# Kernel tuning notes

Hardware: AMD Instinct MI355X
Metric: run time of the kernel (lower is better)

Reference implementation:

```python
import jax, jax.numpy as jnp
import numpy as np

C = 192
B, H, W = 16, 64, 64
FILTERS = (1, 3, 3, 3, 1)
INIT_SCALE = 10.0
LIKELIHOOD_BOUND = 1e-6


def setup_inputs() -> dict:
    key = jax.random.key(0)
    kx, *kb = jax.random.split(key, 6)
    x = jax.random.normal(kx, (B, C, H, W), dtype=jnp.float32)
    scale = INIT_SCALE ** (1.0 / (len(FILTERS) - 1))
    inp = {"x": x}
    for i in range(4):
        init = float(np.log(np.expm1(1.0 / scale / FILTERS[i + 1])))
        inp[f"m{i}"] = jnp.full((C, FILTERS[i + 1], FILTERS[i]), init, dtype=jnp.float32)
        inp[f"b{i}"] = jax.random.uniform(kb[i], (C, FILTERS[i + 1], 1), minval=-0.5, maxval=0.5, dtype=jnp.float32)
    for i in range(3):
        inp[f"f{i}"] = jnp.zeros((C, FILTERS[i + 1], 1), dtype=jnp.float32)
    return inp


def _logits_cumulative(logits, mats, biases, factors):
    # logits: (C, 1, N); mats[i]: (C, f_out, f_in)
    for i in range(len(mats)):
        m = jax.nn.softplus(mats[i])
        logits = jnp.einsum('coi,cin->con', m, logits) + biases[i]
        if i < len(factors):
            logits = logits + jnp.tanh(factors[i]) * jnp.tanh(logits)
    return logits


def reference(x, m0, m1, m2, m3, b0, b1, b2, b3, f0, f1, f2):
    mats = (m0, m1, m2, m3)
    biases = (b0, b1, b2, b3)
    factors = (f0, f1, f2)
    b, c, h, w = x.shape
    xt = jnp.transpose(x, (1, 0, 2, 3)).reshape(c, 1, -1)  # (C,1,N)
    lower = _logits_cumulative(xt - 0.5, mats, biases, factors)
    upper = _logits_cumulative(xt + 0.5, mats, biases, factors)
    sign = jax.lax.stop_gradient(-jnp.sign(lower + upper))
    likelihood = jnp.abs(jax.nn.sigmoid(sign * upper) - jax.nn.sigmoid(sign * lower))
    likelihood = jnp.maximum(likelihood, LIKELIHOOD_BOUND)  # Low_bound forward = clamp
    likelihood = likelihood.reshape(c, b, h, w)
    return jnp.transpose(likelihood, (1, 0, 2, 3))
```

## Files before the change

kernel.cpp:

```cpp
#include <hip/hip_runtime.h>
#include <cmath>

#define NCH 192
#define SLAB 4096
#define LUT_N 512
#define LUT_XMIN (-8.0f)
#define LUT_H (16.0f / (float)LUT_N)
#define LUT_INVH ((float)LUT_N / 16.0f)
#define LUT_OFF (-(LUT_XMIN) * LUT_INVH)
#define SLABS_PER_BLOCK 4

typedef float f4_t __attribute__((ext_vector_type(4)));

__device__ __forceinline__ float sigmoidf_(float x) {
    return 1.0f / (1.0f + __expf(-x));
}

__device__ __forceinline__ float softplusf_(float x) {
    return (x > 20.0f) ? x : log1pf(expf(x));
}

__device__ __forceinline__ float mlp_eval(const float* __restrict__ p, float z,
                                          bool g0, bool g1, bool g2) {
    float t0 = fmaf(p[0], z, p[24]);
    float t1 = fmaf(p[1], z, p[25]);
    float t2 = fmaf(p[2], z, p[26]);
    if (g0) {
        t0 += p[34] * tanhf(t0);
        t1 += p[35] * tanhf(t1);
        t2 += p[36] * tanhf(t2);
    }
    float u0 = fmaf(p[3], t0, fmaf(p[4], t1, fmaf(p[5], t2, p[27])));
    float u1 = fmaf(p[6], t0, fmaf(p[7], t1, fmaf(p[8], t2, p[28])));
    float u2 = fmaf(p[9], t0, fmaf(p[10], t1, fmaf(p[11], t2, p[29])));
    if (g1) {
        u0 += p[37] * tanhf(u0);
        u1 += p[38] * tanhf(u1);
        u2 += p[39] * tanhf(u2);
    }
    float w0 = fmaf(p[12], u0, fmaf(p[13], u1, fmaf(p[14], u2, p[30])));
    float w1 = fmaf(p[15], u0, fmaf(p[16], u1, fmaf(p[17], u2, p[31])));
    float w2 = fmaf(p[18], u0, fmaf(p[19], u1, fmaf(p[20], u2, p[32])));
    if (g2) {
        w0 += p[40] * tanhf(w0);
        w1 += p[41] * tanhf(w1);
        w2 += p[42] * tanhf(w2);
    }
    return fmaf(p[21], w0, fmaf(p[22], w1, fmaf(p[23], w2, p[33])));
}

__device__ __forceinline__ float element(const float* __restrict__ p, float v,
                                         bool g0, bool g1, bool g2) {
    float lo = mlp_eval(p, v - 0.5f, g0, g1, g2);
    float up = mlp_eval(p, v + 0.5f, g0, g1, g2);
    float ssum = lo + up;
    float s = (ssum > 0.0f) ? -1.0f : ((ssum < 0.0f) ? 1.0f : 0.0f);
    float lk = fabsf(sigmoidf_(s * up) - sigmoidf_(s * lo));
    return fmaxf(lk, 1e-6f);
}

__device__ __forceinline__ void stage_params(
    float* p, int c, int tid,
    const float* __restrict__ m0, const float* __restrict__ b0,
    const float* __restrict__ m1, const float* __restrict__ b1,
    const float* __restrict__ m2, const float* __restrict__ b2,
    const float* __restrict__ m3, const float* __restrict__ b3,
    const float* __restrict__ f0, const float* __restrict__ f1,
    const float* __restrict__ f2)
{
    if (tid < 43) {
        float v;
        if (tid < 3)       v = softplusf_(m0[c * 3 + tid]);
        else if (tid < 12) v = softplusf_(m1[c * 9 + (tid - 3)]);
        else if (tid < 21) v = softplusf_(m2[c * 9 + (tid - 12)]);
        else if (tid < 24) v = softplusf_(m3[c * 3 + (tid - 21)]);
        else if (tid < 27) v = b0[c * 3 + (tid - 24)];
        else if (tid < 30) v = b1[c * 3 + (tid - 27)];
        else if (tid < 33) v = b2[c * 3 + (tid - 30)];
        else if (tid < 34) v = b3[c];
        else if (tid < 37) v = tanhf(f0[c * 3 + (tid - 34)]);
        else if (tid < 40) v = tanhf(f1[c * 3 + (tid - 37)]);
        else               v = tanhf(f2[c * 3 + (tid - 40)]);
        p[tid] = v;
    }
}

__global__ __launch_bounds__(256) void eb_fused_kernel(
    const float* __restrict__ x,
    const float* __restrict__ m0, const float* __restrict__ b0,
    const float* __restrict__ m1, const float* __restrict__ b1,
    const float* __restrict__ m2, const float* __restrict__ b2,
    const float* __restrict__ m3, const float* __restrict__ b3,
    const float* __restrict__ f0, const float* __restrict__ f1,
    const float* __restrict__ f2,
    float* __restrict__ out)
{
    __shared__ float p[43];
    __shared__ float f[LUT_N + 1];

    const int c   = blockIdx.x >> 2;
    const int q   = blockIdx.x & 3;
    const int tid = threadIdx.x;

    stage_params(p, c, tid, m0, b0, m1, b1, m2, b2, m3, b3, f0, f1, f2);
    __syncthreads();

    const bool g0 = (p[34] != 0.0f) | (p[35] != 0.0f) | (p[36] != 0.0f);
    const bool g1 = (p[37] != 0.0f) | (p[38] != 0.0f) | (p[39] != 0.0f);
    const bool g2 = (p[40] != 0.0f) | (p[41] != 0.0f) | (p[42] != 0.0f);

    float4 v[SLABS_PER_BLOCK * 4];
    size_t bases[SLABS_PER_BLOCK];
#pragma unroll
    for (int s = 0; s < SLABS_PER_BLOCK; ++s) {
        const int b = q * SLABS_PER_BLOCK + s;
        bases[s] = ((size_t)b * NCH + c) * SLAB;
        const float4* __restrict__ xin = (const float4*)(x + bases[s]);
#pragma unroll
        for (int k = 0; k < 4; ++k) v[s * 4 + k] = xin[tid + k * 256];
    }

    f[tid]       = element(p, fmaf((float)tid,         LUT_H, LUT_XMIN), g0, g1, g2);
    f[tid + 256] = element(p, fmaf((float)(tid + 256), LUT_H, LUT_XMIN), g0, g1, g2);
    if (tid == 0) {
        f[LUT_N] = element(p, fmaf((float)LUT_N, LUT_H, LUT_XMIN), g0, g1, g2);
    }
    __syncthreads();

#pragma unroll
    for (int s = 0; s < SLABS_PER_BLOCK; ++s) {
        f4_t* __restrict__ o = (f4_t*)(out + bases[s]);
#pragma unroll
        for (int k = 0; k < 4; ++k) {
            const float4 vv = v[s * 4 + k];
            f4_t r;
            {
                float t = fmaf(vv.x, LUT_INVH, LUT_OFF);
                t = fminf(fmaxf(t, 0.0f), (float)(LUT_N - 1));
                float tf = floorf(t);
                int i = (int)tf;
                r.x = fmaf(t - tf, f[i + 1] - f[i], f[i]);
            }
            {
                float t = fmaf(vv.y, LUT_INVH, LUT_OFF);
                t = fminf(fmaxf(t, 0.0f), (float)(LUT_N - 1));
                float tf = floorf(t);
                int i = (int)tf;
                r.y = fmaf(t - tf, f[i + 1] - f[i], f[i]);
            }
            {
                float t = fmaf(vv.z, LUT_INVH, LUT_OFF);
                t = fminf(fmaxf(t, 0.0f), (float)(LUT_N - 1));
                float tf = floorf(t);
                int i = (int)tf;
                r.z = fmaf(t - tf, f[i + 1] - f[i], f[i]);
            }
            {
                float t = fmaf(vv.w, LUT_INVH, LUT_OFF);
                t = fminf(fmaxf(t, 0.0f), (float)(LUT_N - 1));
                float tf = floorf(t);
                int i = (int)tf;
                r.w = fmaf(t - tf, f[i + 1] - f[i], f[i]);
            }
            __builtin_nontemporal_store(r, &o[tid + k * 256]);
        }
    }
}

extern "C" void kernel_launch(void* const* d_in, const int* in_sizes, int n_in,
                              void* d_out, int out_size, void* d_ws, size_t ws_size,
                              hipStream_t stream) {
    const float* x = (const float*)d_in[0];
    const float *m0, *m1, *m2, *m3, *b0, *b1, *b2, *b3;
    if (in_sizes[2] == 1728) {
        m0 = (const float*)d_in[1]; m1 = (const float*)d_in[2];
        m2 = (const float*)d_in[3]; m3 = (const float*)d_in[4];
        b0 = (const float*)d_in[5]; b1 = (const float*)d_in[6];
        b2 = (const float*)d_in[7]; b3 = (const float*)d_in[8];
    } else {
        m0 = (const float*)d_in[1]; b0 = (const float*)d_in[2];
        m1 = (const float*)d_in[3]; b1 = (const float*)d_in[4];
        m2 = (const float*)d_in[5]; b2 = (const float*)d_in[6];
        m3 = (const float*)d_in[7]; b3 = (const float*)d_in[8];
    }
    const float* f0 = (const float*)d_in[9];
    const float* f1 = (const float*)d_in[10];
    const float* f2 = (const float*)d_in[11];
    float* out = (float*)d_out;

    const int nblocks = NCH * (16 / SLABS_PER_BLOCK);
    eb_fused_kernel<<<nblocks, 256, 0, stream>>>(x, m0, b0, m1, b1, m2, b2, m3, b3,
                                                 f0, f1, f2, out);
}
```

Baseline: 122.0 us.

## Split LUT build into separate kernel and stream one slab per block

Builds each channel's interpolation table once in a small prologue kernel into workspace, storing value and slope pairs. A second streaming kernel with one slab per block then loads the prebuilt table and interpolates with a single LDS read per element. The intent is to take the MLP table evaluation off the critical path of the bandwidth-bound pass and raise occupancy. The cost is an extra kernel launch and a dependency on workspace being available, with the old fused kernel kept as a fallback.

```diff
diff --git a/kernel.cpp b/kernel.cpp
--- a/kernel.cpp
+++ b/kernel.cpp
@@ -3,14 +3,15 @@
 
 #define NCH 192
 #define SLAB 4096
+#define NB 16
 #define LUT_N 512
 #define LUT_XMIN (-8.0f)
 #define LUT_H (16.0f / (float)LUT_N)
 #define LUT_INVH ((float)LUT_N / 16.0f)
 #define LUT_OFF (-(LUT_XMIN) * LUT_INVH)
-#define SLABS_PER_BLOCK 4
 
 typedef float f4_t __attribute__((ext_vector_type(4)));
+typedef float f2_t __attribute__((ext_vector_type(2)));
 
 __device__ __forceinline__ float sigmoidf_(float x) {
     return 1.0f / (1.0f + __expf(-x));
@@ -85,6 +86,102 @@
     }
 }
 
+__global__ __launch_bounds__(256) void eb_build_kernel(
+    const float* __restrict__ m0, const float* __restrict__ b0,
+    const float* __restrict__ m1, const float* __restrict__ b1,
+    const float* __restrict__ m2, const float* __restrict__ b2,
+    const float* __restrict__ m3, const float* __restrict__ b3,
+    const float* __restrict__ f0, const float* __restrict__ f1,
+    const float* __restrict__ f2,
+    f2_t* __restrict__ lutg)
+{
+    __shared__ float p[43];
+    __shared__ float traw[LUT_N + 1];
+
+    const int c   = blockIdx.x;
+    const int tid = threadIdx.x;
+
+    stage_params(p, c, tid, m0, b0, m1, b1, m2, b2, m3, b3, f0, f1, f2);
+    __syncthreads();
+
+    const bool g0 = (p[34] != 0.0f) | (p[35] != 0.0f) | (p[36] != 0.0f);
+    const bool g1 = (p[37] != 0.0f) | (p[38] != 0.0f) | (p[39] != 0.0f);
+    const bool g2 = (p[40] != 0.0f) | (p[41] != 0.0f) | (p[42] != 0.0f);
+
+    traw[tid]       = element(p, fmaf((float)tid,         LUT_H, LUT_XMIN), g0, g1, g2);
+    traw[tid + 256] = element(p, fmaf((float)(tid + 256), LUT_H, LUT_XMIN), g0, g1, g2);
+    if (tid == 0) {
+        traw[LUT_N] = element(p, fmaf((float)LUT_N, LUT_H, LUT_XMIN), g0, g1, g2);
+    }
+    __syncthreads();
+
+    f2_t e0; e0.x = traw[tid];       e0.y = traw[tid + 1]   - traw[tid];
+    f2_t e1; e1.x = traw[tid + 256]; e1.y = traw[tid + 257] - traw[tid + 256];
+    f2_t* __restrict__ dst = lutg + (size_t)c * LUT_N;
+    dst[tid]       = e0;
+    dst[tid + 256] = e1;
+}
+
+__global__ __launch_bounds__(256, 8) void eb_stream_kernel(
+    const float* __restrict__ x,
+    const f2_t* __restrict__ lutg,
+    float* __restrict__ out)
+{
+    __shared__ f2_t lut[LUT_N];
+
+    const int tid = threadIdx.x;
+    const int c   = blockIdx.x % NCH;
+    const size_t base = (size_t)blockIdx.x * SLAB;
+
+    const f2_t* __restrict__ lg = lutg + (size_t)c * LUT_N;
+    f2_t e0 = lg[tid];
+    f2_t e1 = lg[tid + 256];
+
+    const float4* __restrict__ xin = (const float4*)(x + base);
+    float4 v0 = xin[tid];
+    float4 v1 = xin[tid + 256];
+    float4 v2 = xin[tid + 512];
+    float4 v3 = xin[tid + 768];
+
+    lut[tid]       = e0;
+    lut[tid + 256] = e1;
+    __syncthreads();
+
+    f4_t* __restrict__ o = (f4_t*)(out + base);
+
+#define INTERP(dst, vv)                                            \
+    {                                                              \
+        float t = fmaf((vv), LUT_INVH, LUT_OFF);                   \
+        t = fminf(fmaxf(t, 0.0f), (float)(LUT_N - 1));             \
+        float tf = floorf(t);                                      \
+        int i = (int)tf;                                           \
+        const f2_t e = lut[i];                                     \
+        (dst) = fmaf(t - tf, e.y, e.x);                            \
+    }
+
+    {
+        f4_t r;
+        INTERP(r.x, v0.x) INTERP(r.y, v0.y) INTERP(r.z, v0.z) INTERP(r.w, v0.w)
+        __builtin_nontemporal_store(r, &o[tid]);
+    }
+    {
+        f4_t r;
+        INTERP(r.x, v1.x) INTERP(r.y, v1.y) INTERP(r.z, v1.z) INTERP(r.w, v1.w)
+        __builtin_nontemporal_store(r, &o[tid + 256]);
+    }
+    {
+        f4_t r;
+        INTERP(r.x, v2.x) INTERP(r.y, v2.y) INTERP(r.z, v2.z) INTERP(r.w, v2.w)
+        __builtin_nontemporal_store(r, &o[tid + 512]);
+    }
+    {
+        f4_t r;
+        INTERP(r.x, v3.x) INTERP(r.y, v3.y) INTERP(r.z, v3.z) INTERP(r.w, v3.w)
+        __builtin_nontemporal_store(r, &o[tid + 768]);
+    }
+#undef INTERP
+}
+
 __global__ __launch_bounds__(256) void eb_fused_kernel(
     const float* __restrict__ x,
     const float* __restrict__ m0, const float* __restrict__ b0,
@@ -109,11 +206,11 @@
     const bool g1 = (p[37] != 0.0f) | (p[38] != 0.0f) | (p[39] != 0.0f);
     const bool g2 = (p[40] != 0.0f) | (p[41] != 0.0f) | (p[42] != 0.0f);
 
-    float4 v[SLABS_PER_BLOCK * 4];
-    size_t bases[SLABS_PER_BLOCK];
-#pragma unroll
-    for (int s = 0; s < SLABS_PER_BLOCK; ++s) {
-        const int b = q * SLABS_PER_BLOCK + s;
+    float4 v[16];
+    size_t bases[4];
+#pragma unroll
+    for (int s = 0; s < 4; ++s) {
+        const int b = q * 4 + s;
         bases[s] = ((size_t)b * NCH + c) * SLAB;
         const float4* __restrict__ xin = (const float4*)(x + bases[s]);
 #pragma unroll
@@ -128,7 +225,7 @@
     __syncthreads();
 
 #pragma unroll
-    for (int s = 0; s < SLABS_PER_BLOCK; ++s) {
+    for (int s = 0; s < 4; ++s) {
         f4_t* __restrict__ o = (f4_t*)(out + bases[s]);
 #pragma unroll
         for (int k = 0; k < 4; ++k) {
@@ -137,29 +234,25 @@
             {
                 float t = fmaf(vv.x, LUT_INVH, LUT_OFF);
                 t = fminf(fmaxf(t, 0.0f), (float)(LUT_N - 1));
-                float tf = floorf(t);
-                int i = (int)tf;
+                float tf = floorf(t); int i = (int)tf;
                 r.x = fmaf(t - tf, f[i + 1] - f[i], f[i]);
             }
             {
                 float t = fmaf(vv.y, LUT_INVH, LUT_OFF);
                 t = fminf(fmaxf(t, 0.0f), (float)(LUT_N - 1));
-                float tf = floorf(t);
-                int i = (int)tf;
+                float tf = floorf(t); int i = (int)tf;
                 r.y = fmaf(t - tf, f[i + 1] - f[i], f[i]);
             }
             {
                 float t = fmaf(vv.z, LUT_INVH, LUT_OFF);
                 t = fminf(fmaxf(t, 0.0f), (float)(LUT_N - 1));
-                float tf = floorf(t);
-                int i = (int)tf;
+                float tf = floorf(t); int i = (int)tf;
                 r.z = fmaf(t - tf, f[i + 1] - f[i], f[i]);
             }
             {
                 float t = fmaf(vv.w, LUT_INVH, LUT_OFF);
                 t = fminf(fmaxf(t, 0.0f), (float)(LUT_N - 1));
-                float tf = floorf(t);
-                int i = (int)tf;
+                float tf = floorf(t); int i = (int)tf;
                 r.w = fmaf(t - tf, f[i + 1] - f[i], f[i]);
             }
             __builtin_nontemporal_store(r, &o[tid + k * 256]);
@@ -188,7 +281,14 @@
     const float* f2 = (const float*)d_in[11];
     float* out = (float*)d_out;
 
-    const int nblocks = NCH * (16 / SLABS_PER_BLOCK);
-    eb_fused_kernel<<<nblocks, 256, 0, stream>>>(x, m0, b0, m1, b1, m2, b2, m3, b3,
-                                                 f0, f1, f2, out);
-}
+    const size_t lut_bytes = (size_t)NCH * LUT_N * sizeof(f2_t);
+    if (d_ws != nullptr && ws_size >= lut_bytes) {
+        f2_t* lutg = (f2_t*)d_ws;
+        eb_build_kernel<<<NCH, 256, 0, stream>>>(m0, b0, m1, b1, m2, b2, m3, b3,
+                                                 f0, f1, f2, lutg);
+        eb_stream_kernel<<<NB * NCH, 256, 0, stream>>>(x, lutg, out);
+    } else {
+        eb_fused_kernel<<<NCH * 4, 256, 0, stream>>>(x, m0, b0, m1, b1, m2, b2,
+                                                     m3, b3, f0, f1, f2, out);
+    }
+}
```

Result: slower. 125.1 us (+2.5%).
